# Optimization experiments

Measured on AMD Instinct MI355X. Metric: run time of the kernel, lower is better.

The kernel has to match this reference:

```python
import jax, jax.numpy as jnp
import numpy as np

NUM_HEADS = 8

B, N, M = 2, 10000, 320000
QD = KD = HD = 256


def setup_inputs() -> dict:
    key = jax.random.key(0)
    k1, k2, k3, k4, k5 = jax.random.split(key, 5)
    x_q = jax.random.normal(k1, (B, N, QD), dtype=jnp.float32)
    x_k = jax.random.normal(k2, (B, N, KD), dtype=jnp.float32)
    mask = jax.random.randint(k3, (2, M), 0, N, dtype=jnp.int64)
    # xavier_uniform: limit = sqrt(6/(fan_in+fan_out))
    lim_q = float(np.sqrt(6.0 / (QD + HD)))
    lim_k = float(np.sqrt(6.0 / (KD + HD)))
    w_q = jax.random.uniform(k4, (QD, HD), minval=-lim_q, maxval=lim_q, dtype=jnp.float32)
    w_k = jax.random.uniform(k5, (KD, HD), minval=-lim_k, maxval=lim_k, dtype=jnp.float32)
    return {"x_q": x_q, "x_k": x_k, "mask": mask, "w_q": w_q, "w_k": w_k}


def reference(x_q, x_k, mask, w_q, w_k):
    b, n, _ = x_q.shape
    m = mask.shape[1]
    d = w_q.shape[1]          # hidden_dim
    h = NUM_HEADS
    dh = d // h
    q = x_q @ w_q             # (b, n, d)
    k = x_k @ w_k             # (b, n, d)
    # edge gather + elementwise multiply
    prod = q[:, mask[0], :] * k[:, mask[1], :]            # (b, m, d)
    # head buffer is i // (d/h): contiguous blocks -> reshape-sum
    a = prod.reshape(b, m, h, dh).sum(axis=-1)            # (b, m, h)
    a = a / jnp.sqrt(jnp.float32(w_k.shape[0]))           # / sqrt(key_dim)
    # segment softmax over destination index = mask[1 - reduce_dim], reduce_dim=1 -> mask[0]
    idx = mask[0]
    a = a - a.max()                                       # global max, as in source
    e = jnp.exp(a)                                        # (b, m, h)
    seg = jnp.zeros((b, n, h), e.dtype).at[:, idx, :].add(e)
    return e / (seg[:, idx, :] + 1e-16)
```

## Files before the change

### kernel.cpp

```cpp
#include <hip/hip_runtime.h>
#include <hip/hip_bf16.h>
#include <hip/hip_fp16.h>

#define DHID 256
#define NHEAD 8
#define BATCH 2

typedef _Float16 h8 __attribute__((ext_vector_type(8)));
typedef float f4 __attribute__((ext_vector_type(4)));

__global__ __launch_bounds__(256) void transpose_w(
    const float* __restrict__ Wq, const float* __restrict__ Wk,
    _Float16* __restrict__ Wtq, _Float16* __restrict__ Wtk)
{
    const float* W = blockIdx.z ? Wk : Wq;
    _Float16* Wt   = blockIdx.z ? Wtk : Wtq;
    __shared__ float tile[32][33];
    const int tx = threadIdx.x;
    const int ty = threadIdx.y;
    const int n0 = blockIdx.x * 32;
    const int k0 = blockIdx.y * 32;
#pragma unroll
    for (int j = 0; j < 32; j += 8)
        tile[ty + j][tx] = W[(size_t)(k0 + ty + j) * DHID + n0 + tx];
    __syncthreads();
#pragma unroll
    for (int j = 0; j < 32; j += 8)
        Wt[(size_t)(n0 + ty + j) * DHID + k0 + tx] = (_Float16)tile[tx][ty + j];
}

__global__ __launch_bounds__(256, 2) void gemm_mfma(
    const float* __restrict__ Xq, const float* __restrict__ Xk,
    const _Float16* __restrict__ Wtq, const _Float16* __restrict__ Wtk,
    _Float16* __restrict__ Qh, _Float16* __restrict__ Kh, int Mrows)
{
    const float* X       = blockIdx.z ? Xk : Xq;
    const _Float16* Wt   = blockIdx.z ? Wtk : Wtq;
    _Float16* C          = blockIdx.z ? Kh : Qh;

    __shared__ _Float16 As[64 * 256];
    __shared__ _Float16 Bs[64 * 256];

    const int t    = threadIdx.x;
    const int lane = t & 63;
    const int wave = t >> 6;
    const int rowBase = blockIdx.x * 64;

#pragma unroll
    for (int i = 0; i < 8; ++i) {
        int idx = t + i * 256;
        int row = idx >> 5;
        int c   = idx & 31;
        int grow = rowBase + row;
        f4 v0 = {0,0,0,0}, v1 = {0,0,0,0};
        if (grow < Mrows) {
            const float* p = X + (size_t)grow * DHID + c * 8;
            v0 = *(const f4*)p;
            v1 = *(const f4*)(p + 4);
        }
        h8 hv;
        hv[0]=(_Float16)v0[0]; hv[1]=(_Float16)v0[1]; hv[2]=(_Float16)v0[2]; hv[3]=(_Float16)v0[3];
        hv[4]=(_Float16)v1[0]; hv[5]=(_Float16)v1[1]; hv[6]=(_Float16)v1[2]; hv[7]=(_Float16)v1[3];
        int sc = c ^ (row & 7);
        *(h8*)&As[row * 256 + sc * 8] = hv;
    }

    const int ar   = wave * 16 + (lane & 15);
    const int quad = lane >> 4;

    for (int ct64 = 0; ct64 < 4; ++ct64) {
#pragma unroll
        for (int i = 0; i < 8; ++i) {
            int idx = t + i * 256;
            int n = idx >> 5;
            int c = idx & 31;
            h8 hv = *(const h8*)(Wt + (size_t)(ct64 * 64 + n) * DHID + c * 8);
            int sc = c ^ (n & 7);
            *(h8*)&Bs[n * 256 + sc * 8] = hv;
        }
        __syncthreads();

        f4 acc[4] = {{0,0,0,0},{0,0,0,0},{0,0,0,0},{0,0,0,0}};
#pragma unroll
        for (int kc = 0; kc < 8; ++kc) {
            int ac = (kc * 4 + quad) ^ (ar & 7);
            h8 afrag = *(const h8*)&As[ar * 256 + ac * 8];
#pragma unroll
            for (int ct = 0; ct < 4; ++ct) {
                int bn = ct * 16 + (lane & 15);
                int bc = (kc * 4 + quad) ^ (bn & 7);
                h8 bfrag = *(const h8*)&Bs[bn * 256 + bc * 8];
                acc[ct] = __builtin_amdgcn_mfma_f32_16x16x32_f16(afrag, bfrag, acc[ct], 0, 0, 0);
            }
        }

#pragma unroll
        for (int ct = 0; ct < 4; ++ct) {
#pragma unroll
            for (int r = 0; r < 4; ++r) {
                int grow = rowBase + wave * 16 + quad * 4 + r;
                if (grow < Mrows)
                    C[(size_t)grow * DHID + ct64 * 64 + ct * 16 + (lane & 15)] = (_Float16)acc[ct][r];
            }
        }
        __syncthreads();
    }
}

__global__ __launch_bounds__(256) void edge_kernel(
    const _Float16* __restrict__ Qh, const _Float16* __restrict__ Kh,
    const int* __restrict__ mask, float* __restrict__ out,
    float* __restrict__ seg, int M, int N)
{
    const int lane = threadIdx.x & 63;
    const int wave = threadIdx.x >> 6;
    const int g = lane >> 3;
    const int h = lane & 7;
    const long e0 = ((long)blockIdx.x * 4 + wave) * 8;
    const int b = blockIdx.y;
    if (e0 >= M) return;

    int idxv = 0;
    {
        long le = e0 + (lane & 7);
        if (le >= M) le = M - 1;
        if (lane < 8)       idxv = mask[le];
        else if (lane < 16) idxv = mask[M + le];
    }
    const int src = __shfl(idxv, g);
    const int dst = __shfl(idxv, 8 + g);

    const _Float16* qp = Qh + ((size_t)b * N + src) * DHID + h * 32;
    const _Float16* kp = Kh + ((size_t)b * N + dst) * DHID + h * 32;
    float s = 0.f;
#pragma unroll
    for (int j = 0; j < 4; ++j) {
        h8 qv = *(const h8*)(qp + j * 8);
        h8 kv = *(const h8*)(kp + j * 8);
#pragma unroll
        for (int u = 0; u < 8; ++u)
            s += (float)qv[u] * (float)kv[u];
    }
    const long e = e0 + g;
    if (e < M) {
        float ev = expf(s * 0.0625f);
        out[((size_t)b * M + e) * NHEAD + h] = ev;
        atomicAdd(seg + ((size_t)b * N + src) * NHEAD + h, ev);
    }
}

__global__ __launch_bounds__(256) void norm_kernel(
    const int* __restrict__ mask, const float* __restrict__ seg,
    float* __restrict__ out, int M, int N, int BM)
{
    int idx = blockIdx.x * 256 + threadIdx.x;
    if (idx >= BM) return;
    int b = idx / M;
    int e = idx - b * M;
    int src = mask[e];
    const float4* s4 = (const float4*)(seg + ((size_t)b * N + src) * NHEAD);
    float4 s0 = s4[0], s1 = s4[1];
    float4* o4 = (float4*)(out + (size_t)idx * NHEAD);
    float4 o0 = o4[0], o1 = o4[1];
    o0.x /= (s0.x + 1e-16f); o0.y /= (s0.y + 1e-16f);
    o0.z /= (s0.z + 1e-16f); o0.w /= (s0.w + 1e-16f);
    o1.x /= (s1.x + 1e-16f); o1.y /= (s1.y + 1e-16f);
    o1.z /= (s1.z + 1e-16f); o1.w /= (s1.w + 1e-16f);
    o4[0] = o0; o4[1] = o1;
}

extern "C" void kernel_launch(void* const* d_in, const int* in_sizes, int n_in,
                              void* d_out, int out_size, void* d_ws, size_t ws_size,
                              hipStream_t stream) {
    const float* x_q  = (const float*)d_in[0];
    const float* x_k  = (const float*)d_in[1];
    const int*   mask = (const int*)d_in[2];
    const float* w_q  = (const float*)d_in[3];
    const float* w_k  = (const float*)d_in[4];
    float* out = (float*)d_out;

    const int M = in_sizes[2] / 2;
    const int N = in_sizes[0] / (BATCH * DHID);
    const int Mrows = BATCH * N;

    _Float16* Qh  = (_Float16*)d_ws;
    _Float16* Kh  = Qh  + (size_t)Mrows * DHID;
    _Float16* Wtq = Kh  + (size_t)Mrows * DHID;
    _Float16* Wtk = Wtq + (size_t)DHID * DHID;
    float*    seg = (float*)(Wtk + (size_t)DHID * DHID);

    hipMemsetAsync(seg, 0, (size_t)BATCH * N * NHEAD * sizeof(float), stream);

    dim3 tgrid(DHID / 32, DHID / 32, 2);
    transpose_w<<<tgrid, dim3(32, 8), 0, stream>>>(w_q, w_k, Wtq, Wtk);

    dim3 ggrid((Mrows + 63) / 64, 1, 2);
    gemm_mfma<<<ggrid, 256, 0, stream>>>(x_q, x_k, Wtq, Wtk, Qh, Kh, Mrows);

    int waves = (M + 7) / 8;
    dim3 egrid((waves + 3) / 4, BATCH);
    edge_kernel<<<egrid, 256, 0, stream>>>(Qh, Kh, mask, out, seg, M, N);

    const int BM = BATCH * M;
    norm_kernel<<<(BM + 255) / 256, 256, 0, stream>>>(mask, seg, out, M, N, BM);
}
```

Baseline: 185.2 us.

## Restructure edge gather to full-row loads, fuse seg memset into prep kernel

The edge kernel now has each half-wave read a full 512-byte Q/K row, each lane taking 8 halves, for four edge pairs at once. This replaces per-head 64-byte strided reads and issues all gathers up front for memory-level parallelism. Head sums are reduced with two xor-shuffles, and outputs use nontemporal stores with an occupancy hint. The seg memset is folded into the weight-transpose launch to save one launch, and norm uses fast reciprocal multiplies with nontemporal stores, which may cost slight precision.

```diff
diff --git a/kernel.cpp b/kernel.cpp
--- a/kernel.cpp
+++ b/kernel.cpp
@@ -9,10 +9,16 @@
 typedef _Float16 h8 __attribute__((ext_vector_type(8)));
 typedef float f4 __attribute__((ext_vector_type(4)));
 
-__global__ __launch_bounds__(256) void transpose_w(
+__global__ __launch_bounds__(256) void prep_kernel(
     const float* __restrict__ Wq, const float* __restrict__ Wk,
-    _Float16* __restrict__ Wtq, _Float16* __restrict__ Wtk)
-{
+    _Float16* __restrict__ Wtq, _Float16* __restrict__ Wtk,
+    float* __restrict__ seg, int segN)
+{
+    if (blockIdx.z == 2) {
+        int idx = (blockIdx.x * 8 + blockIdx.y) * 256 + threadIdx.y * 32 + threadIdx.x;
+        for (int i = idx; i < segN; i += 64 * 256) seg[i] = 0.f;
+        return;
+    }
     const float* W = blockIdx.z ? Wk : Wq;
     _Float16* Wt   = blockIdx.z ? Wtk : Wtq;
     __shared__ float tile[32][33];
@@ -107,15 +113,16 @@
     }
 }
 
-__global__ __launch_bounds__(256) void edge_kernel(
+__global__ __launch_bounds__(256, 6) void edge_kernel(
     const _Float16* __restrict__ Qh, const _Float16* __restrict__ Kh,
     const int* __restrict__ mask, float* __restrict__ out,
     float* __restrict__ seg, int M, int N)
 {
     const int lane = threadIdx.x & 63;
     const int wave = threadIdx.x >> 6;
-    const int g = lane >> 3;
-    const int h = lane & 7;
+    const int c    = lane & 31;
+    const int half = lane >> 5;
+    const int h    = c >> 2;
     const long e0 = ((long)blockIdx.x * 4 + wave) * 8;
     const int b = blockIdx.y;
     if (e0 >= M) return;
@@ -127,25 +134,38 @@
         if (lane < 8)       idxv = mask[le];
         else if (lane < 16) idxv = mask[M + le];
     }
-    const int src = __shfl(idxv, g);
-    const int dst = __shfl(idxv, 8 + g);
-
-    const _Float16* qp = Qh + ((size_t)b * N + src) * DHID + h * 32;
-    const _Float16* kp = Kh + ((size_t)b * N + dst) * DHID + h * 32;
-    float s = 0.f;
-#pragma unroll
-    for (int j = 0; j < 4; ++j) {
-        h8 qv = *(const h8*)(qp + j * 8);
-        h8 kv = *(const h8*)(kp + j * 8);
+
+    const _Float16* Qb = Qh + (size_t)b * N * DHID;
+    const _Float16* Kb = Kh + (size_t)b * N * DHID;
+
+    int sidx[4], didx[4];
+#pragma unroll
+    for (int p = 0; p < 4; ++p) {
+        sidx[p] = __shfl(idxv, p * 2 + half);
+        didx[p] = __shfl(idxv, 8 + p * 2 + half);
+    }
+
+    h8 qv[4], kv[4];
+#pragma unroll
+    for (int p = 0; p < 4; ++p) {
+        qv[p] = *(const h8*)(Qb + (size_t)sidx[p] * DHID + c * 8);
+        kv[p] = *(const h8*)(Kb + (size_t)didx[p] * DHID + c * 8);
+    }
+
+#pragma unroll
+    for (int p = 0; p < 4; ++p) {
+        float s = 0.f;
 #pragma unroll
         for (int u = 0; u < 8; ++u)
-            s += (float)qv[u] * (float)kv[u];
-    }
-    const long e = e0 + g;
-    if (e < M) {
+            s += (float)qv[p][u] * (float)kv[p][u];
+        s += __shfl_xor(s, 1);
+        s += __shfl_xor(s, 2);
         float ev = expf(s * 0.0625f);
-        out[((size_t)b * M + e) * NHEAD + h] = ev;
-        atomicAdd(seg + ((size_t)b * N + src) * NHEAD + h, ev);
+        const long e = e0 + p * 2 + half;
+        if ((c & 3) == 0 && e < M) {
+            __builtin_nontemporal_store(ev, &out[((size_t)b * M + e) * NHEAD + h]);
+            atomicAdd(seg + ((size_t)b * N + sidx[p]) * NHEAD + h, ev);
+        }
     }
 }
 
@@ -158,15 +178,20 @@
     int b = idx / M;
     int e = idx - b * M;
     int src = mask[e];
-    const float4* s4 = (const float4*)(seg + ((size_t)b * N + src) * NHEAD);
-    float4 s0 = s4[0], s1 = s4[1];
-    float4* o4 = (float4*)(out + (size_t)idx * NHEAD);
-    float4 o0 = o4[0], o1 = o4[1];
-    o0.x /= (s0.x + 1e-16f); o0.y /= (s0.y + 1e-16f);
-    o0.z /= (s0.z + 1e-16f); o0.w /= (s0.w + 1e-16f);
-    o1.x /= (s1.x + 1e-16f); o1.y /= (s1.y + 1e-16f);
-    o1.z /= (s1.z + 1e-16f); o1.w /= (s1.w + 1e-16f);
-    o4[0] = o0; o4[1] = o1;
+    const f4* s4 = (const f4*)(seg + ((size_t)b * N + src) * NHEAD);
+    f4 s0 = s4[0], s1 = s4[1];
+    f4* o4 = (f4*)(out + (size_t)idx * NHEAD);
+    f4 o0 = o4[0], o1 = o4[1];
+    o0[0] *= __builtin_amdgcn_rcpf(s0[0] + 1e-16f);
+    o0[1] *= __builtin_amdgcn_rcpf(s0[1] + 1e-16f);
+    o0[2] *= __builtin_amdgcn_rcpf(s0[2] + 1e-16f);
+    o0[3] *= __builtin_amdgcn_rcpf(s0[3] + 1e-16f);
+    o1[0] *= __builtin_amdgcn_rcpf(s1[0] + 1e-16f);
+    o1[1] *= __builtin_amdgcn_rcpf(s1[1] + 1e-16f);
+    o1[2] *= __builtin_amdgcn_rcpf(s1[2] + 1e-16f);
+    o1[3] *= __builtin_amdgcn_rcpf(s1[3] + 1e-16f);
+    __builtin_nontemporal_store(o0, &o4[0]);
+    __builtin_nontemporal_store(o1, &o4[1]);
 }
 
 extern "C" void kernel_launch(void* const* d_in, const int* in_sizes, int n_in,
@@ -189,16 +214,14 @@
     _Float16* Wtk = Wtq + (size_t)DHID * DHID;
     float*    seg = (float*)(Wtk + (size_t)DHID * DHID);
 
-    hipMemsetAsync(seg, 0, (size_t)BATCH * N * NHEAD * sizeof(float), stream);
-
-    dim3 tgrid(DHID / 32, DHID / 32, 2);
-    transpose_w<<<tgrid, dim3(32, 8), 0, stream>>>(w_q, w_k, Wtq, Wtk);
+    prep_kernel<<<dim3(DHID / 32, DHID / 32, 3), dim3(32, 8), 0, stream>>>(
+        w_q, w_k, Wtq, Wtk, seg, BATCH * N * NHEAD);
 
     dim3 ggrid((Mrows + 63) / 64, 1, 2);
     gemm_mfma<<<ggrid, 256, 0, stream>>>(x_q, x_k, Wtq, Wtk, Qh, Kh, Mrows);
 
-    int waves = (M + 7) / 8;
-    dim3 egrid((waves + 3) / 4, BATCH);
+    long waves = (M + 7) / 8;
+    dim3 egrid((unsigned)((waves + 3) / 4), BATCH);
     edge_kernel<<<egrid, 256, 0, stream>>>(Qh, Kh, mask, out, seg, M, N);
 
     const int BM = BATCH * M;
```

New measurement: 181.6 us. About the same (-1.9%).
